# Optimization experiments

Hardware: AMD Instinct MI355X
Metric: run time of the kernel (lower is better)

## Reference

```python
import jax, jax.numpy as jnp
import numpy as np

H, NOPE, ROPE, VD, KV_LORA, HID = 16, 128, 64, 128, 512, 2048
QK = NOPE + ROPE
SCALE = QK ** -0.5
EPS = 1e-5


def _rope(x, freqs):
    # x: [b, t, h, ROPE]; freqs: [t, ROPE//2] angles. Complex-pair rotation.
    cos = jnp.cos(freqs)[None, :, None, :]
    sin = jnp.sin(freqs)[None, :, None, :]
    xr = x.reshape(x.shape[:-1] + (ROPE // 2, 2))
    x1, x2 = xr[..., 0], xr[..., 1]
    o1 = x1 * cos - x2 * sin
    o2 = x1 * sin + x2 * cos
    return jnp.stack([o1, o2], axis=-1).reshape(x.shape)


def _layernorm(x, g, b):
    mu = jnp.mean(x, axis=-1, keepdims=True)
    var = jnp.var(x, axis=-1, keepdims=True)
    return (x - mu) * jax.lax.rsqrt(var + EPS) * g + b


def setup_inputs() -> dict:
    key = jax.random.key(0)
    ks = jax.random.split(key, 6)
    b, t = 2, 2048

    def xavier(k, shape):
        fan_in, fan_out = shape
        lim = np.sqrt(6.0 / (fan_in + fan_out))
        return jax.random.uniform(k, shape, jnp.float32, -lim, lim)

    hidden_states = jax.random.normal(ks[0], (b, t, HID), jnp.float32)
    # rope angles: theta_i = 10000^(-2i/ROPE), angle[p,i] = p * theta_i
    inv_freq = 1.0 / (10000.0 ** (np.arange(0, ROPE, 2, dtype=np.float32) / ROPE))
    freqs = jnp.asarray(np.arange(t, dtype=np.float32)[:, None] * inv_freq[None, :])
    # causal additive mask broadcastable to [b,t,s,h]
    causal = jnp.where(jnp.arange(t)[None, :] <= jnp.arange(t)[:, None], 0.0, -1e9)
    attention_mask = causal.astype(jnp.float32)[None, :, :, None]
    return {
        "hidden_states": hidden_states,
        "freqs": freqs,
        "attention_mask": attention_mask,
        "Wq": xavier(ks[1], (HID, H * QK)),
        "Wkv_a": xavier(ks[2], (HID, KV_LORA + ROPE)),
        "kv_gamma": jnp.ones((KV_LORA,), jnp.float32),
        "kv_beta": jnp.zeros((KV_LORA,), jnp.float32),
        "Wkv_b": xavier(ks[3], (KV_LORA, H * (NOPE + VD))),
        "Wout": xavier(ks[4], (H * VD, HID)),
    }


def reference(hidden_states, freqs, attention_mask, Wq, Wkv_a, kv_gamma, kv_beta, Wkv_b, Wout):
    b, t, _ = hidden_states.shape
    # Q projection -> [b,t,H,QK], split nope/rope, rotate rope part
    q = (hidden_states @ Wq).reshape(b, t, H, QK)
    q_nope, q_rope = q[..., :NOPE], q[..., NOPE:]
    q_rope = _rope(q_rope, freqs)
    # compressed KV latent + shared rope key
    kv = hidden_states @ Wkv_a                      # [b,t,KV_LORA+ROPE]
    kv_lat, k_rope = kv[..., :KV_LORA], kv[..., KV_LORA:]
    k_rope = _rope(k_rope[:, :, None, :], freqs)    # [b,t,1,ROPE]
    kv_lat = _layernorm(kv_lat, kv_gamma, kv_beta)
    kvb = (kv_lat @ Wkv_b).reshape(b, t, H, NOPE + VD)
    k_nope, v = kvb[..., :NOPE], kvb[..., NOPE:]
    k = jnp.concatenate([k_nope, jnp.broadcast_to(k_rope, (b, t, H, ROPE))], axis=-1)
    q = jnp.concatenate([q_nope, q_rope], axis=-1)
    # scores [b,t,s,h]; NOTE: source applies softmax over dim=-1 == HEAD axis (faithful)
    scores = jnp.einsum("bthd,bshd->btsh", q, k) * SCALE + attention_mask
    weights = jax.nn.softmax(scores.astype(jnp.float32), axis=-1).astype(q.dtype)
    attn = jnp.einsum("btsh,bshd->bthd", weights, v).reshape(b, t, H * VD)
    return attn @ Wout
```

## Files before the change

kernel.cpp:

```cpp
#include <hip/hip_runtime.h>

typedef unsigned short u16;
typedef short bf16x8 __attribute__((ext_vector_type(8)));
typedef float f32x4 __attribute__((ext_vector_type(4)));
typedef float f32x16 __attribute__((ext_vector_type(16)));
typedef unsigned short u16x8 __attribute__((ext_vector_type(8)));

#define GLOBAL_AS __attribute__((address_space(1)))
#define LDS_AS __attribute__((address_space(3)))
#define DEVINL __device__ __forceinline__

#define BATCH 2
#define TSEQ 2048
#define NHEAD 16
#define QK 192
#define VD 128
#define HID 2048
#define MROWS 4096
#define SCALE_QK 0.07216878364870323f

DEVINL float b2f(u16 u) { union { unsigned i; float f; } x; x.i = ((unsigned)u) << 16; return x.f; }
DEVINL u16 f2b(float f) {
    union { float f; unsigned u; } x; x.f = f;
    unsigned r = x.u + 0x7fffu + ((x.u >> 16) & 1u);
    return (u16)(r >> 16);
}
DEVINL void gload_lds16(const u16* g, u16* l) {
    __builtin_amdgcn_global_load_lds((const GLOBAL_AS unsigned*)g, (LDS_AS unsigned*)l, 16, 0, 0);
}
DEVINL unsigned pk2(float a, float b) {
    unsigned d;
    asm("v_cvt_pk_bf16_f32 %0, %1, %2" : "=v"(d) : "v"(a), "v"(b));
    return d;
}


__global__ void cvt_bf16x8(const float* __restrict__ in, u16* __restrict__ out, int n8) {
    int i = blockIdx.x * 256 + threadIdx.x;
    if (i < n8) {
        const float4* p = (const float4*)(in + (size_t)i * 8);
        float4 x = p[0], y = p[1];
        u16x8 o;
        o[0] = f2b(x.x); o[1] = f2b(x.y); o[2] = f2b(x.z); o[3] = f2b(x.w);
        o[4] = f2b(y.x); o[5] = f2b(y.y); o[6] = f2b(y.z); o[7] = f2b(y.w);
        *(u16x8*)(out + (size_t)i * 8) = o;
    }
}

__global__ void rope_tab_k(const float* __restrict__ freqs, float2* __restrict__ tab) {
    int i = blockIdx.x * 256 + threadIdx.x;
    float f = freqs[i], s, c;
    sincosf(f, &s, &c);
    tab[i] = make_float2(c, s);
}

__global__ void transpose_cvt(const float* __restrict__ in, u16* __restrict__ out,
                              int R, int C, int Cpad) {
    __shared__ float tile[32][33];
    int c0 = blockIdx.x * 32, r0 = blockIdx.y * 32;
    int tx = threadIdx.x, ty = threadIdx.y;
#pragma unroll
    for (int j = 0; j < 4; j++) {
        int r = r0 + ty + j * 8, c = c0 + tx;
        tile[ty + j * 8][tx] = (c < C) ? in[(size_t)r * C + c] : 0.f;
    }
    __syncthreads();
#pragma unroll
    for (int j = 0; j < 4; j++) {
        int oc = c0 + ty + j * 8;
        int orr = r0 + tx;
        if (oc < Cpad) out[(size_t)oc * R + orr] = f2b(tile[tx][ty + j * 8]);
    }
}

template<int MODE>
__global__ __launch_bounds__(256)
void gemm_bt(const u16* __restrict__ A, const u16* __restrict__ BT, int Kdim,
             void* __restrict__ out0, void* __restrict__ out1, void* __restrict__ out2,
             const float2* __restrict__ tab) {
    __shared__ __align__(16) u16 As[128 * 32];
    __shared__ __align__(16) u16 Bs[128 * 32];
    const int tid = threadIdx.x, lane = tid & 63, wave = tid >> 6;
    const int m0 = blockIdx.x * 128, n0 = blockIdx.y * 128;
    const int wr = wave >> 1, wc = wave & 1;

    f32x4 acc[4][4];
#pragma unroll
    for (int i = 0; i < 4; i++)
#pragma unroll
        for (int j = 0; j < 4; j++) acc[i][j] = f32x4{0.f, 0.f, 0.f, 0.f};

    const int e0 = (wave * 2 + 0) * 512 + lane * 8;
    const int e1 = (wave * 2 + 1) * 512 + lane * 8;
    const u16* gA0 = A + (size_t)(m0 + (e0 >> 5)) * Kdim + (e0 & 31);
    const u16* gA1 = A + (size_t)(m0 + (e1 >> 5)) * Kdim + (e1 & 31);
    const u16* gB0 = BT + (size_t)(n0 + (e0 >> 5)) * Kdim + (e0 & 31);
    const u16* gB1 = BT + (size_t)(n0 + (e1 >> 5)) * Kdim + (e1 & 31);
    u16* lA0 = &As[(wave * 2 + 0) * 512];
    u16* lA1 = &As[(wave * 2 + 1) * 512];
    u16* lB0 = &Bs[(wave * 2 + 0) * 512];
    u16* lB1 = &Bs[(wave * 2 + 1) * 512];

    const int arow = lane & 15, koff = (lane >> 4) * 8;

    for (int k0 = 0; k0 < Kdim; k0 += 32) {
        gload_lds16(gA0, lA0); gload_lds16(gA1, lA1);
        gload_lds16(gB0, lB0); gload_lds16(gB1, lB1);
        gA0 += 32; gA1 += 32; gB0 += 32; gB1 += 32;
        asm volatile("s_waitcnt vmcnt(0)" ::: "memory");
        __syncthreads();
        bf16x8 af[4], bfr[4];
#pragma unroll
        for (int i = 0; i < 4; i++)
            af[i] = *(const bf16x8*)&As[(wr * 64 + i * 16 + arow) * 32 + koff];
#pragma unroll
        for (int j = 0; j < 4; j++)
            bfr[j] = *(const bf16x8*)&Bs[(wc * 64 + j * 16 + arow) * 32 + koff];
#pragma unroll
        for (int i = 0; i < 4; i++)
#pragma unroll
            for (int j = 0; j < 4; j++)
                acc[i][j] = __builtin_amdgcn_mfma_f32_16x16x32_bf16(af[i], bfr[j], acc[i][j], 0, 0, 0);
        __syncthreads();
    }

#pragma unroll
    for (int i = 0; i < 4; i++)
#pragma unroll
        for (int j = 0; j < 4; j++)
#pragma unroll
            for (int r = 0; r < 4; r++) {
                int row = m0 + wr * 64 + i * 16 + (lane >> 4) * 4 + r;
                int col = n0 + wc * 64 + j * 16 + (lane & 15);
                float v = acc[i][j][r];
                if constexpr (MODE == 0) {
                    int h = col / 192, d = col % 192;
                    int b = row >> 11, t = row & 2047;
                    float vv = v;
                    float pv = __shfl_xor(v, 1);
                    if (d >= 128) {
                        float2 cs = tab[t * 32 + ((d - 128) >> 1)];
                        vv = v * cs.x + pv * ((lane & 1) ? cs.y : -cs.y);
                    }
                    ((u16*)out0)[((size_t)(b * 16 + h) * 2048 + t) * 192 + d] = f2b(vv);
                } else if constexpr (MODE == 1) {
                    ((float*)out0)[(size_t)row * 640 + col] = v;
                } else if constexpr (MODE == 2) {
                    int h = col >> 8, d = col & 255;
                    int b = row >> 11, t = row & 2047;
                    size_t base = (size_t)(b * 16 + h) * 2048 + t;
                    if (d < 128) ((u16*)out0)[base * 192 + d] = f2b(v);
                    else {
                        u16 bv = f2b(v);
                        ((u16*)out1)[base * 128 + (d - 128)] = bv;
                        ((u16*)out2)[((size_t)(b * 16 + h) * 128 + (d - 128)) * 2048 + t] = bv;
                    }
                } else {
                    ((float*)out0)[(size_t)row * 2048 + col] = v;
                }
            }
}

__global__ __launch_bounds__(256)
void ln_krope(const float* __restrict__ kvf, const float* __restrict__ gamma,
              const float* __restrict__ beta, const float2* __restrict__ tab,
              u16* __restrict__ kvlat, u16* __restrict__ kbuf) {
    int row = blockIdx.x, tid = threadIdx.x;
    const float* x = kvf + (size_t)row * 640;
    float v0 = x[tid], v1 = x[tid + 256];
    float s = v0 + v1, sq = v0 * v0 + v1 * v1;
#pragma unroll
    for (int off = 1; off < 64; off <<= 1) { s += __shfl_xor(s, off); sq += __shfl_xor(sq, off); }
    __shared__ float ssum[4], ssq[4];
    if ((tid & 63) == 0) { ssum[tid >> 6] = s; ssq[tid >> 6] = sq; }
    __syncthreads();
    s = ssum[0] + ssum[1] + ssum[2] + ssum[3];
    sq = ssq[0] + ssq[1] + ssq[2] + ssq[3];
    float mu = s * (1.f / 512.f);
    float var = sq * (1.f / 512.f) - mu * mu;
    float rs = rsqrtf(var + 1e-5f);
    kvlat[(size_t)row * 512 + tid] = f2b((v0 - mu) * rs * gamma[tid] + beta[tid]);
    kvlat[(size_t)row * 512 + tid + 256] = f2b((v1 - mu) * rs * gamma[tid + 256] + beta[tid + 256]);
    if (tid < 32) {
        int t = row & 2047, b = row >> 11;
        float x1 = x[512 + 2 * tid], x2 = x[512 + 2 * tid + 1];
        float2 cs = tab[t * 32 + tid];
        u16 u1 = f2b(x1 * cs.x - x2 * cs.y), u2 = f2b(x1 * cs.y + x2 * cs.x);
        for (int h = 0; h < 16; ++h) {
            size_t base = ((size_t)(b * 16 + h) * 2048 + t) * 192 + 128 + 2 * tid;
            kbuf[base] = u1; kbuf[base + 1] = u2;
        }
    }
}

__global__ void suff1(const u16* __restrict__ vbuf, float* __restrict__ psum) {
    int bh = blockIdx.x, c = blockIdx.y, d = threadIdx.x;
    float s = 0.f;
    const u16* vp = vbuf + ((size_t)bh * 2048 + c * 128) * 128 + d;
    for (int tt = 0; tt < 128; ++tt) s += b2f(vp[(size_t)tt * 128]);
    psum[((size_t)bh * 16 + c) * 128 + d] = s;
}
__global__ void suff2(const float* __restrict__ psum, float* __restrict__ csuf) {
    int bh = blockIdx.x, d = threadIdx.x;
    float run = 0.f;
    for (int c = 15; c >= 0; --c) {
        csuf[((size_t)bh * 16 + c) * 128 + d] = run;
        run += psum[((size_t)bh * 16 + c) * 128 + d];
    }
}
__global__ void suff3(const u16* __restrict__ vbuf, const float* __restrict__ csuf,
                      u16* __restrict__ attnb) {
    int bh = blockIdx.x, c = blockIdx.y, d = threadIdx.x;
    int b = bh >> 4, h = bh & 15;
    float run = csuf[((size_t)bh * 16 + c) * 128 + d];
    for (int tt = 127; tt >= 0; --tt) {
        int t = c * 128 + tt;
        attnb[((size_t)b * 2048 + t) * 2048 + h * 128 + d] = f2b(run * 0.0625f);
        run += b2f(vbuf[((size_t)bh * 2048 + t) * 128 + d]);
    }
}

__global__ __launch_bounds__(256, 3)
void z_kernel(const u16* __restrict__ qbuf, const u16* __restrict__ kbuf,
              u16* __restrict__ zbufT) {
    __shared__ __align__(16) u16 Ks[2 * 12288];
    const int tid = threadIdx.x, lane = tid & 63, wave = tid >> 6;
    const int hi = lane >> 5, l31 = lane & 31;
    const int tgrp = wave & 1, sblk = wave >> 1;
    int id = blockIdx.x;
    int b = id & 1, p = id >> 1;
    int tT = (int)((sqrtf(8.f * (float)p + 1.f) - 1.f) * 0.5f);
    while ((tT + 1) * (tT + 2) / 2 <= p) ++tT;
    while (tT * (tT + 1) / 2 > p) --tT;
    int sT = p - tT * (tT + 1) / 2;
    const int t0 = tT * 64, s0 = sT * 64;
    const int rK = sblk * 32 + l31;
    const int t_loc = tgrp * 32 + l31;

    float zacc[16];
#pragma unroll
    for (int r = 0; r < 16; r++) zacc[r] = 0.f;

    bf16x8 qA[12];
    auto QLOAD = [&](int h) {
        const u16* qp = qbuf + ((size_t)(b * 16 + h) * 2048 + t0 + t_loc) * 192 + hi * 8;
#pragma unroll
        for (int kk = 0; kk < 12; kk++) qA[kk] = *(const bf16x8*)(qp + kk * 16);
    };
    auto KSTAGE = [&](int h, int bi) {
        const size_t hrow = (size_t)(b * 16 + h) * 2048;
#pragma unroll
        for (int j = 0; j < 6; j++) {
            int idx = (wave * 6 + j) * 64 + lane;
            int rr2 = idx / 24, cc = idx % 24, cs = cc ^ (rr2 & 7);
            gload_lds16(kbuf + (hrow + s0 + rr2) * 192 + cs * 8, &Ks[bi * 12288 + idx * 8]);
        }
    };
    auto COMPUTE = [&](const u16* K) {
        f32x16 e;
#pragma unroll
        for (int r = 0; r < 16; r++) e[r] = 0.f;
        __builtin_amdgcn_s_setprio(1);
#pragma unroll
        for (int kk = 0; kk < 12; kk++) {
            int slot = (2 * kk + hi) ^ (rK & 7);
            bf16x8 kf = *(const bf16x8*)&K[rK * 192 + slot * 8];
            e = __builtin_amdgcn_mfma_f32_32x32x16_bf16(kf, qA[kk], e, 0, 0, 0);
        }
        __builtin_amdgcn_s_setprio(0);
#pragma unroll
        for (int r = 0; r < 16; r++) zacc[r] += __expf(e[r] * SCALE_QK);
    };

    QLOAD(0);
    KSTAGE(0, 0);
    asm volatile("s_waitcnt vmcnt(0)" ::: "memory");
    __builtin_amdgcn_s_barrier();
#pragma unroll 1
    for (int h = 0; h < 16; ++h) {
        int cur = h & 1;
        if (h < 15) {
            KSTAGE(h + 1, cur ^ 1);
            asm volatile("s_waitcnt vmcnt(18)" ::: "memory");
        } else {
            asm volatile("s_waitcnt vmcnt(12)" ::: "memory");
        }
        __builtin_amdgcn_s_barrier();
        __builtin_amdgcn_sched_barrier(0);
        COMPUTE(&Ks[cur * 12288]);
        __builtin_amdgcn_s_barrier();
        if (h < 15) QLOAD(h + 1);
    }
#pragma unroll
    for (int r = 0; r < 16; r++) {
        int spat = (r & 3) + 8 * (r >> 2) + 4 * hi;
        int sg = s0 + sblk * 32 + spat;
        zbufT[((size_t)b * 2048 + sg) * 2048 + t0 + t_loc] = f2b(__fdividef(1.f, zacc[r]));
    }
}

__global__ __launch_bounds__(512, 1)
void attn_pv(const u16* __restrict__ qbuf, const u16* __restrict__ kbuf,
             const u16* __restrict__ vtbuf, const u16* __restrict__ zbufT,
             u16* __restrict__ attnb) {
    __shared__ __align__(16) u16 lds[57344];
    u16* Ks = lds;
    u16* Vt = lds + 24576;
    u16* Zs = lds + 40960;
    const int tid = threadIdx.x, lane = tid & 63, wave = tid >> 6;
    const int hi = lane >> 5, l31 = lane & 31;
    const int tgrp = wave & 3, sblk = wave >> 2;
    int id = blockIdx.x;
    int xcd = id & 7, j2 = id >> 3;
    int pr = j2 & 7, g = j2 >> 3;
    int bh = xcd * 4 + g;
    const int b = bh >> 4, h = bh & 15;
    const size_t kvrow = (size_t)bh * 2048;
    const int rK = sblk * 32 + l31;
    const int t_loc = tgrp * 32 + l31;
    const int zg = t_loc >> 3, zoff = t_loc & 7;

    for (int part = 0; part < 2; ++part) {
        const int T = part ? (15 - pr) : pr;
        const int t0p = T * 128, nst = 2 * T + 2;
        const int tg = t0p + t_loc;

        bf16x8 qf[12];
        {
            const u16* qp = qbuf + (kvrow + tg) * 192 + hi * 8;
#pragma unroll
            for (int kk = 0; kk < 12; kk++) qf[kk] = *(const bf16x8*)(qp + kk * 16);
        }
        f32x16 o[4];
#pragma unroll
        for (int db = 0; db < 4; db++)
#pragma unroll
            for (int r = 0; r < 16; r++) o[db][r] = 0.f;

        auto STAGE = [&](int st, int bi) {
            const int s0 = st * 64;
#pragma unroll
            for (int j = 0; j < 3; j++) {
                int idx = (wave * 3 + j) * 64 + lane;
                int rr2 = idx / 24, cc = idx % 24, cs = cc ^ (rr2 & 7);
                gload_lds16(kbuf + (kvrow + s0 + rr2) * 192 + cs * 8, &Ks[bi * 12288 + idx * 8]);
            }
#pragma unroll
            for (int j = 0; j < 2; j++) {
                int idx = (wave * 2 + j) * 64 + lane;
                int d = idx >> 3, cc = idx & 7, cs = cc ^ (d & 7);
                gload_lds16(vtbuf + ((size_t)bh * 128 + d) * 2048 + s0 + cs * 8, &Vt[bi * 8192 + idx * 8]);
            }
#pragma unroll
            for (int j = 0; j < 2; j++) {
                int idx = (wave * 2 + j) * 64 + lane;
                int sr = idx >> 4, cc = idx & 15, cs = cc ^ (sr & 15);
                gload_lds16(zbufT + ((size_t)b * 2048 + s0 + sr) * 2048 + t0p + cs * 8, &Zs[bi * 8192 + idx * 8]);
            }
        };
        STAGE(0, 0);
        for (int st = 0; st < nst; ++st) {
            int cur = st & 1;
            if (st + 1 < nst) {
                STAGE(st + 1, cur ^ 1);
                asm volatile("s_waitcnt vmcnt(7)" ::: "memory");
            } else {
                asm volatile("s_waitcnt vmcnt(0)" ::: "memory");
            }
            __builtin_amdgcn_s_barrier();
            __builtin_amdgcn_sched_barrier(0);
            const u16* Kc = &Ks[cur * 12288];
            const u16* Vc = &Vt[cur * 8192];
            const u16* Zc = &Zs[cur * 8192];
            f32x16 sacc;
#pragma unroll
            for (int r = 0; r < 16; r++) sacc[r] = 0.f;
            __builtin_amdgcn_s_setprio(1);
#pragma unroll
            for (int kk = 0; kk < 12; kk++) {
                int slot = (2 * kk + hi) ^ (rK & 7);
                bf16x8 kf = *(const bf16x8*)&Kc[rK * 192 + slot * 8];
                sacc = __builtin_amdgcn_mfma_f32_32x32x16_bf16(kf, qf[kk], sacc, 0, 0, 0);
            }
            __builtin_amdgcn_s_setprio(0);
            const int s0g = st * 64 + sblk * 32;
            float w[16];
#pragma unroll
            for (int r = 0; r < 16; r++) {
                int spat = (r & 3) + 8 * (r >> 2) + 4 * hi;
                int sr = sblk * 32 + spat;
                float rz = b2f(Zc[sr * 128 + ((zg ^ (sr & 15)) << 3) + zoff]);
                w[r] = (s0g + spat <= tg) ? __expf(sacc[r] * SCALE_QK) * rz : 0.f;
            }
            unsigned pw0 = pk2(w[0], w[1]), pw1 = pk2(w[2], w[3]);
            unsigned pw2 = pk2(w[4], w[5]), pw3 = pk2(w[6], w[7]);
            unsigned pw4 = pk2(w[8], w[9]), pw5 = pk2(w[10], w[11]);
            unsigned pw6 = pk2(w[12], w[13]), pw7 = pk2(w[14], w[15]);
            unsigned a0 = pw0, a1 = pw1, a2 = pw4, a3 = pw5;
            asm volatile("v_permlane32_swap_b32 %0, %1" : "+v"(a0), "+v"(pw2));
            asm volatile("v_permlane32_swap_b32 %0, %1" : "+v"(a1), "+v"(pw3));
            asm volatile("v_permlane32_swap_b32 %0, %1" : "+v"(a2), "+v"(pw6));
            asm volatile("v_permlane32_swap_b32 %0, %1" : "+v"(a3), "+v"(pw7));
            union PU { unsigned u[4]; bf16x8 v; } p0, p1;
            p0.u[0] = a0;  p0.u[1] = a1;  p0.u[2] = pw2; p0.u[3] = pw3;
            p1.u[0] = a2;  p1.u[1] = a3;  p1.u[2] = pw6; p1.u[3] = pw7;
            __builtin_amdgcn_s_setprio(1);
#pragma unroll
            for (int db = 0; db < 4; db++) {
                int dv = db * 32 + l31;
#pragma unroll
                for (int ks = 0; ks < 2; ks++) {
                    int slot = (sblk * 4 + 2 * ks + hi) ^ (dv & 7);
                    bf16x8 vb = *(const bf16x8*)&Vc[dv * 64 + slot * 8];
                    o[db] = __builtin_amdgcn_mfma_f32_32x32x16_bf16(ks ? p1.v : p0.v, vb, o[db], 0, 0, 0);
                }
            }
            __builtin_amdgcn_s_setprio(0);
            __builtin_amdgcn_s_barrier();
        }
        __syncthreads();
        float* red = (float*)lds;
        if (sblk == 0) {
#pragma unroll
            for (int db = 0; db < 4; db++)
#pragma unroll
                for (int r = 0; r < 16; r++) {
                    int trow = (r & 3) + 8 * (r >> 2) + 4 * hi;
                    red[(tgrp * 32 + trow) * 128 + db * 32 + l31] = o[db][r];
                }
        }
        __syncthreads();
        if (sblk == 1) {
#pragma unroll
            for (int db = 0; db < 4; db++)
#pragma unroll
                for (int r = 0; r < 16; r++) {
                    int trow = (r & 3) + 8 * (r >> 2) + 4 * hi;
                    float val = o[db][r] + red[(tgrp * 32 + trow) * 128 + db * 32 + l31];
                    size_t oi = ((size_t)b * 2048 + t0p + tgrp * 32 + trow) * 2048 + h * 128 + db * 32 + l31;
                    attnb[oi] = f2b(val + b2f(attnb[oi]));
                }
        }
        __syncthreads();
    }
}

extern "C" void kernel_launch(void* const* d_in, const int* in_sizes, int n_in,
                              void* d_out, int out_size, void* d_ws, size_t ws_size,
                              hipStream_t stream) {
    (void)in_sizes; (void)n_in; (void)out_size;
    const float* hidden = (const float*)d_in[0];
    const float* freqs  = (const float*)d_in[1];
    const float* Wq     = (const float*)d_in[3];
    const float* Wkva   = (const float*)d_in[4];
    const float* gamma  = (const float*)d_in[5];
    const float* beta   = (const float*)d_in[6];
    const float* Wkvb   = (const float*)d_in[7];
    const float* Wout   = (const float*)d_in[8];
    float* outp = (float*)d_out;

    char* ws = (char*)d_ws;
    size_t off = 0;
    auto alloc = [&](size_t bytes) -> void* {
        void* p = ws + off; off += (bytes + 255) & ~(size_t)255; return p;
    };
    u16*   hid_b = (u16*)alloc((size_t)MROWS * HID * 2);
    u16*   WqT   = (u16*)alloc((size_t)3072 * 2048 * 2);
    u16*   WkvaT = (u16*)alloc((size_t)640 * 2048 * 2);
    u16*   WkvbT = (u16*)alloc((size_t)4096 * 512 * 2);
    u16*   WoutT = (u16*)alloc((size_t)2048 * 2048 * 2);
    u16*   qbuf  = (u16*)alloc((size_t)BATCH * NHEAD * TSEQ * QK * 2);
    float* kvf   = (float*)alloc((size_t)MROWS * 640 * 4);
    u16*   kvlat = (u16*)alloc((size_t)MROWS * 512 * 2);
    u16*   kbuf  = (u16*)alloc((size_t)BATCH * NHEAD * TSEQ * QK * 2);
    u16*   vbuf  = (u16*)alloc((size_t)BATCH * NHEAD * TSEQ * VD * 2);
    u16*   attnb = (u16*)alloc((size_t)MROWS * 2048 * 2);
    float2* ropetab = (float2*)alloc((size_t)2048 * 32 * 8);
    float* psum  = (float*)alloc((size_t)32 * 16 * 128 * 4);
    float* csuf  = (float*)alloc((size_t)32 * 16 * 128 * 4);
    if (off > ws_size) return;
    u16* zbufT = WqT;
    u16* vtbuf = hid_b;

    cvt_bf16x8<<<4096, 256, 0, stream>>>(hidden, hid_b, MROWS * HID / 8);
    rope_tab_k<<<256, 256, 0, stream>>>(freqs, ropetab);
    dim3 tb(32, 8);
    transpose_cvt<<<dim3(96, 64), tb, 0, stream>>>(Wq, WqT, 2048, 3072, 3072);
    transpose_cvt<<<dim3(20, 64), tb, 0, stream>>>(Wkva, WkvaT, 2048, 576, 640);
    transpose_cvt<<<dim3(128, 16), tb, 0, stream>>>(Wkvb, WkvbT, 512, 4096, 4096);
    transpose_cvt<<<dim3(64, 64), tb, 0, stream>>>(Wout, WoutT, 2048, 2048, 2048);

    gemm_bt<1><<<dim3(32, 5), 256, 0, stream>>>(hid_b, WkvaT, 2048, kvf, nullptr, nullptr, nullptr);
    gemm_bt<0><<<dim3(32, 24), 256, 0, stream>>>(hid_b, WqT, 2048, qbuf, nullptr, nullptr, ropetab);
    ln_krope<<<MROWS, 256, 0, stream>>>(kvf, gamma, beta, ropetab, kvlat, kbuf);
    gemm_bt<2><<<dim3(32, 32), 256, 0, stream>>>(kvlat, WkvbT, 512, kbuf, vbuf, vtbuf, nullptr);

    suff1<<<dim3(32, 16), 128, 0, stream>>>(vbuf, psum);
    suff2<<<32, 128, 0, stream>>>(psum, csuf);
    suff3<<<dim3(32, 16), 128, 0, stream>>>(vbuf, csuf, attnb);

    z_kernel<<<1056, 256, 0, stream>>>(qbuf, kbuf, zbufT);
    attn_pv<<<256, 512, 0, stream>>>(qbuf, kbuf, vtbuf, zbufT, attnb);

    gemm_bt<3><<<dim3(32, 16), 256, 0, stream>>>(attnb, WoutT, 2048, outp, nullptr, nullptr, nullptr);
}
```

Baseline: 536.3 us.

## Triple-buffer K/V prefetch in attn_pv and remap z_kernel tile order

attn_pv now splits staging into a K/V part and a Z part. K/V tiles are prefetched two stages ahead into a three-slot ring in LDS, while Z stays double-buffered, with vmcnt waits adjusted to match. This is meant to hide more global-load latency behind the QK and PV MFMAs, at the cost of raising LDS use to about 152 KB per block. Separately, z_kernel remaps block ids so consecutive triangular tiles land on the same XCD/batch group, aiming for better L2 reuse of Q and K rows.

```diff
diff --git a/kernel.cpp b/kernel.cpp
--- a/kernel.cpp
+++ b/kernel.cpp
@@ -228,7 +228,10 @@
     const int hi = lane >> 5, l31 = lane & 31;
     const int tgrp = wave & 1, sblk = wave >> 1;
     int id = blockIdx.x;
-    int b = id & 1, p = id >> 1;
+    int b = id & 1;
+    int q4 = (id >> 1) & 3;
+    int j = id >> 3;
+    int p = q4 * 132 + j;
     int tT = (int)((sqrtf(8.f * (float)p + 1.f) - 1.f) * 0.5f);
     while ((tT + 1) * (tT + 2) / 2 <= p) ++tT;
     while (tT * (tT + 1) / 2 > p) --tT;
@@ -250,8 +253,8 @@
     auto KSTAGE = [&](int h, int bi) {
         const size_t hrow = (size_t)(b * 16 + h) * 2048;
 #pragma unroll
-        for (int j = 0; j < 6; j++) {
-            int idx = (wave * 6 + j) * 64 + lane;
+        for (int j2 = 0; j2 < 6; j2++) {
+            int idx = (wave * 6 + j2) * 64 + lane;
             int rr2 = idx / 24, cc = idx % 24, cs = cc ^ (rr2 & 7);
             gload_lds16(kbuf + (hrow + s0 + rr2) * 192 + cs * 8, &Ks[bi * 12288 + idx * 8]);
         }
@@ -303,10 +306,10 @@
 void attn_pv(const u16* __restrict__ qbuf, const u16* __restrict__ kbuf,
              const u16* __restrict__ vtbuf, const u16* __restrict__ zbufT,
              u16* __restrict__ attnb) {
-    __shared__ __align__(16) u16 lds[57344];
+    __shared__ __align__(16) u16 lds[77824];
     u16* Ks = lds;
-    u16* Vt = lds + 24576;
-    u16* Zs = lds + 40960;
+    u16* Vt = lds + 36864;
+    u16* Zs = lds + 61440;
     const int tid = threadIdx.x, lane = tid & 63, wave = tid >> 6;
     const int hi = lane >> 5, l31 = lane & 31;
     const int tgrp = wave & 3, sblk = wave >> 2;
@@ -337,7 +340,7 @@
 #pragma unroll
             for (int r = 0; r < 16; r++) o[db][r] = 0.f;
 
-        auto STAGE = [&](int st, int bi) {
+        auto STAGE_KV = [&](int st, int bi) {
             const int s0 = st * 64;
 #pragma unroll
             for (int j = 0; j < 3; j++) {
@@ -351,6 +354,9 @@
                 int d = idx >> 3, cc = idx & 7, cs = cc ^ (d & 7);
                 gload_lds16(vtbuf + ((size_t)bh * 128 + d) * 2048 + s0 + cs * 8, &Vt[bi * 8192 + idx * 8]);
             }
+        };
+        auto STAGE_Z = [&](int st, int bi) {
+            const int s0 = st * 64;
 #pragma unroll
             for (int j = 0; j < 2; j++) {
                 int idx = (wave * 2 + j) * 64 + lane;
@@ -358,20 +364,27 @@
                 gload_lds16(zbufT + ((size_t)b * 2048 + s0 + sr) * 2048 + t0p + cs * 8, &Zs[bi * 8192 + idx * 8]);
             }
         };
-        STAGE(0, 0);
+        STAGE_Z(0, 0);
+        STAGE_KV(0, 0);
+        STAGE_KV(1, 1);
+        int rb = 0;
         for (int st = 0; st < nst; ++st) {
-            int cur = st & 1;
-            if (st + 1 < nst) {
-                STAGE(st + 1, cur ^ 1);
+            int cz = st & 1;
+            if (st + 2 < nst) {
+                STAGE_Z(st + 1, cz ^ 1);
+                STAGE_KV(st + 2, rb == 0 ? 2 : rb - 1);
+                asm volatile("s_waitcnt vmcnt(12)" ::: "memory");
+            } else if (st + 1 < nst) {
+                STAGE_Z(st + 1, cz ^ 1);
                 asm volatile("s_waitcnt vmcnt(7)" ::: "memory");
             } else {
                 asm volatile("s_waitcnt vmcnt(0)" ::: "memory");
             }
             __builtin_amdgcn_s_barrier();
             __builtin_amdgcn_sched_barrier(0);
-            const u16* Kc = &Ks[cur * 12288];
-            const u16* Vc = &Vt[cur * 8192];
-            const u16* Zc = &Zs[cur * 8192];
+            const u16* Kc = &Ks[rb * 12288];
+            const u16* Vc = &Vt[rb * 8192];
+            const u16* Zc = &Zs[cz * 8192];
             f32x16 sacc;
 #pragma unroll
             for (int r = 0; r < 16; r++) sacc[r] = 0.f;
@@ -417,6 +430,7 @@
             }
             __builtin_amdgcn_s_setprio(0);
             __builtin_amdgcn_s_barrier();
+            rb = (rb == 2) ? 0 : rb + 1;
         }
         __syncthreads();
         float* red = (float*)lds;
```

Result: no change. 540.2 us (+0.7%).

## Process two key tiles per z_kernel block to reuse Q fragments

Applied to the files above, without the earlier changes.

Each z_kernel block now handles up to two adjacent 64-key s-tiles for the same query tile, so the Q registers loaded per head serve two K tiles. The grid shrinks from 1056 to 544 blocks, and the pipeline alternates K staging between the two tiles within each head iteration. This cuts redundant Q global loads and per-block overhead. The cost is two accumulators held in registers, more complex wait counts, and fewer blocks, which leaves uneven work per block.

```diff
diff --git a/kernel.cpp b/kernel.cpp
--- a/kernel.cpp
+++ b/kernel.cpp
@@ -229,17 +229,13 @@
     const int tgrp = wave & 1, sblk = wave >> 1;
     int id = blockIdx.x;
     int b = id & 1, p = id >> 1;
-    int tT = (int)((sqrtf(8.f * (float)p + 1.f) - 1.f) * 0.5f);
-    while ((tT + 1) * (tT + 2) / 2 <= p) ++tT;
-    while (tT * (tT + 1) / 2 > p) --tT;
-    int sT = p - tT * (tT + 1) / 2;
-    const int t0 = tT * 64, s0 = sT * 64;
+    int tT = 0;
+    for (;;) { int cnt = (tT + 2) >> 1; if (p < cnt) break; p -= cnt; ++tT; }
+    const int g2 = p * 2;
+    const int ns = ((tT + 1 - g2) >= 2) ? 2 : 1;
+    const int t0 = tT * 64;
     const int rK = sblk * 32 + l31;
     const int t_loc = tgrp * 32 + l31;
-
-    float zacc[16];
-#pragma unroll
-    for (int r = 0; r < 16; r++) zacc[r] = 0.f;
 
     bf16x8 qA[12];
     auto QLOAD = [&](int h) {
@@ -247,16 +243,20 @@
 #pragma unroll
         for (int kk = 0; kk < 12; kk++) qA[kk] = *(const bf16x8*)(qp + kk * 16);
     };
-    auto KSTAGE = [&](int h, int bi) {
+    auto KSTAGE = [&](int h, int st, int bi) {
         const size_t hrow = (size_t)(b * 16 + h) * 2048;
-#pragma unroll
-        for (int j = 0; j < 6; j++) {
-            int idx = (wave * 6 + j) * 64 + lane;
+        const int s0 = st * 64;
+#pragma unroll
+        for (int j2 = 0; j2 < 6; j2++) {
+            int idx = (wave * 6 + j2) * 64 + lane;
             int rr2 = idx / 24, cc = idx % 24, cs = cc ^ (rr2 & 7);
             gload_lds16(kbuf + (hrow + s0 + rr2) * 192 + cs * 8, &Ks[bi * 12288 + idx * 8]);
         }
     };
-    auto COMPUTE = [&](const u16* K) {
+    f32x16 za0, za1;
+#pragma unroll
+    for (int r = 0; r < 16; r++) { za0[r] = 0.f; za1[r] = 0.f; }
+    auto COMPUTE = [&](f32x16& za, const u16* K) {
         f32x16 e;
 #pragma unroll
         for (int r = 0; r < 16; r++) e[r] = 0.f;
@@ -269,33 +269,58 @@
         }
         __builtin_amdgcn_s_setprio(0);
 #pragma unroll
-        for (int r = 0; r < 16; r++) zacc[r] += __expf(e[r] * SCALE_QK);
+        for (int r = 0; r < 16; r++) za[r] += __expf(e[r] * SCALE_QK);
     };
 
     QLOAD(0);
-    KSTAGE(0, 0);
+    KSTAGE(0, g2, 0);
     asm volatile("s_waitcnt vmcnt(0)" ::: "memory");
     __builtin_amdgcn_s_barrier();
+    int kb = 0;
 #pragma unroll 1
     for (int h = 0; h < 16; ++h) {
-        int cur = h & 1;
-        if (h < 15) {
-            KSTAGE(h + 1, cur ^ 1);
-            asm volatile("s_waitcnt vmcnt(18)" ::: "memory");
+        if (ns == 2)      KSTAGE(h, g2 + 1, kb ^ 1);
+        else if (h < 15)  KSTAGE(h + 1, g2, kb ^ 1);
+        if (ns == 2 || h < 15) {
+            if (h > 0) { asm volatile("s_waitcnt vmcnt(18)" ::: "memory"); }
+            else       { asm volatile("s_waitcnt vmcnt(6)"  ::: "memory"); }
         } else {
             asm volatile("s_waitcnt vmcnt(12)" ::: "memory");
         }
         __builtin_amdgcn_s_barrier();
         __builtin_amdgcn_sched_barrier(0);
-        COMPUTE(&Ks[cur * 12288]);
+        COMPUTE(za0, &Ks[kb * 12288]);
         __builtin_amdgcn_s_barrier();
-        if (h < 15) QLOAD(h + 1);
+        if (ns == 1 && h < 15) QLOAD(h + 1);
+        kb ^= 1;
+        if (ns == 2) {
+            if (h < 15) {
+                KSTAGE(h + 1, g2, kb ^ 1);
+                asm volatile("s_waitcnt vmcnt(6)" ::: "memory");
+            } else {
+                asm volatile("s_waitcnt vmcnt(0)" ::: "memory");
+            }
+            __builtin_amdgcn_s_barrier();
+            __builtin_amdgcn_sched_barrier(0);
+            COMPUTE(za1, &Ks[kb * 12288]);
+            __builtin_amdgcn_s_barrier();
+            if (h < 15) QLOAD(h + 1);
+            kb ^= 1;
+        }
     }
 #pragma unroll
     for (int r = 0; r < 16; r++) {
         int spat = (r & 3) + 8 * (r >> 2) + 4 * hi;
-        int sg = s0 + sblk * 32 + spat;
-        zbufT[((size_t)b * 2048 + sg) * 2048 + t0 + t_loc] = f2b(__fdividef(1.f, zacc[r]));
+        int sg = g2 * 64 + sblk * 32 + spat;
+        zbufT[((size_t)b * 2048 + sg) * 2048 + t0 + t_loc] = f2b(__fdividef(1.f, za0[r]));
+    }
+    if (ns == 2) {
+#pragma unroll
+        for (int r = 0; r < 16; r++) {
+            int spat = (r & 3) + 8 * (r >> 2) + 4 * hi;
+            int sg = (g2 + 1) * 64 + sblk * 32 + spat;
+            zbufT[((size_t)b * 2048 + sg) * 2048 + t0 + t_loc] = f2b(__fdividef(1.f, za1[r]));
+        }
     }
 }
 
@@ -499,7 +524,7 @@
     suff2<<<32, 128, 0, stream>>>(psum, csuf);
     suff3<<<dim3(32, 16), 128, 0, stream>>>(vbuf, csuf, attnb);
 
-    z_kernel<<<1056, 256, 0, stream>>>(qbuf, kbuf, zbufT);
+    z_kernel<<<544, 256, 0, stream>>>(qbuf, kbuf, zbufT);
     attn_pv<<<256, 512, 0, stream>>>(qbuf, kbuf, vtbuf, zbufT, attnb);
 
     gemm_bt<3><<<dim3(32, 16), 256, 0, stream>>>(attnb, WoutT, 2048, outp, nullptr, nullptr, nullptr);
```

After: 514.1 us. 4.1% less time.
